# Optimization experiments

Measured on AMD Instinct MI355X. Metric: run time of the kernel, lower is better.

Reference implementation:

```python
import jax, jax.numpy as jnp
import numpy as np

B, H, L, P = 16, 256, 4096, 64  # batch, d_input, seq len (= kernel_size), d_state
R_MIN, R_MAX = 0.9, 1.0         # strong_stability, weak_stability (discrete reservoir radii)


def _as_complex(x):
    # torch.view_as_complex equivalent: trailing dim 2 = (real, imag)
    return x[..., 0] + 1j * x[..., 1]


def setup_inputs() -> dict:
    key = jax.random.key(0)
    ks = jax.random.split(key, 6)
    u = jax.random.normal(ks[0], (B, H, L), jnp.float32)
    C = jax.random.normal(ks[1], (H, P, 2), jnp.float32)       # complex (H,P) as view_as_real
    D = jax.random.normal(ks[2], (H, H), jnp.float32)
    B_bar = jax.random.normal(ks[3], (P, H, 2), jnp.float32)   # complex (P,H) as view_as_real
    # DiscreteStateReservoir: eigenvalues with |lambda| in [strong, weak), uniform phase
    radius = jax.random.uniform(ks[4], (P,), jnp.float32, R_MIN, R_MAX)
    theta = jax.random.uniform(ks[5], (P,), jnp.float32, 0.0, 2.0 * np.pi)
    Lambda_bar = jnp.stack([radius * jnp.cos(theta), radius * jnp.sin(theta)], axis=-1)
    powers = jnp.arange(L, dtype=jnp.float32)
    return {"u": u, "C": C, "D": D, "B_bar": B_bar, "Lambda_bar": Lambda_bar, "powers": powers}


def reference(u, C, D, B_bar, Lambda_bar, powers):
    Cc = _as_complex(C)            # (H, P) complex64
    Bc = _as_complex(B_bar)        # (P, H) complex64
    Lc = _as_complex(Lambda_bar)   # (P,)   complex64
    # Vandermonde: (P, L) = Lambda_bar[p] ** powers[l]
    vand = Lc[:, None] ** powers[None, :]
    # einsum('hp,ph->hp') is elementwise C[h,p]*B_bar[p,h]; then contract over p
    kernel = jnp.einsum('hp,pl->hl', Cc * Bc.T, vand)            # (H, L) complex64
    # circular FFT convolution along L
    y = jnp.fft.ifft(jnp.fft.fft(u, axis=-1) * jnp.fft.fft(kernel, axis=-1)[None], axis=-1)
    # einsum('hh,bhl->bhl', D, u) uses only diag(D)
    y = y.real + jnp.diagonal(D)[None, :, None] * u
    return jnp.tanh(y)
```

## Files before the change

### kernel.cpp

```cpp
#include <hip/hip_runtime.h>
#include <cmath>

#define NF 4096
#define PI2F 6.2831853071795864769f

typedef float2 cf;

__device__ __forceinline__ cf cmulf(cf a, cf b){
  return make_float2(fmaf(a.x, b.x, -(a.y*b.y)), fmaf(a.x, b.y, a.y*b.x));
}
__device__ __forceinline__ cf cadd(cf a, cf b){ return make_float2(a.x+b.x, a.y+b.y); }
__device__ __forceinline__ cf csub(cf a, cf b){ return make_float2(a.x-b.x, a.y-b.y); }

__device__ __forceinline__ int phys(int i){ return i + (i >> 3); }

__device__ __forceinline__ int rev8(int i){
  return ((i & 7) << 9) | (((i >> 3) & 7) << 6) | (((i >> 6) & 7) << 3) | ((i >> 9) & 7);
}

template<int INV>
__device__ __forceinline__ void dft8(cf* v){
  const float HF = 0.7071067811865476f;
  cf e0,e1,e2,e3,o0,o1,o2,o3;
  {
    cf t0 = cadd(v[0], v[4]);
    cf t1 = csub(v[0], v[4]);
    cf t2 = cadd(v[2], v[6]);
    cf t3 = csub(v[2], v[6]);
    e0 = cadd(t0,t2); e2 = csub(t0,t2);
    if (!INV){ e1 = make_float2(t1.x+t3.y, t1.y-t3.x); e3 = make_float2(t1.x-t3.y, t1.y+t3.x); }
    else     { e1 = make_float2(t1.x-t3.y, t1.y+t3.x); e3 = make_float2(t1.x+t3.y, t1.y-t3.x); }
  }
  {
    cf t0 = cadd(v[1], v[5]);
    cf t1 = csub(v[1], v[5]);
    cf t2 = cadd(v[3], v[7]);
    cf t3 = csub(v[3], v[7]);
    o0 = cadd(t0,t2); o2 = csub(t0,t2);
    if (!INV){ o1 = make_float2(t1.x+t3.y, t1.y-t3.x); o3 = make_float2(t1.x-t3.y, t1.y+t3.x); }
    else     { o1 = make_float2(t1.x-t3.y, t1.y+t3.x); o3 = make_float2(t1.x+t3.y, t1.y-t3.x); }
  }
  cf w1, w2, w3;
  if (!INV){
    w1 = make_float2(HF*(o1.x + o1.y), HF*(o1.y - o1.x));
    w2 = make_float2(o2.y, -o2.x);
    w3 = make_float2(HF*(o3.y - o3.x), -HF*(o3.x + o3.y));
  } else {
    w1 = make_float2(HF*(o1.x - o1.y), HF*(o1.y + o1.x));
    w2 = make_float2(-o2.y, o2.x);
    w3 = make_float2(-HF*(o3.x + o3.y), HF*(o3.x - o3.y));
  }
  v[0] = cadd(e0,o0); v[4] = csub(e0,o0);
  v[1] = cadd(e1,w1); v[5] = csub(e1,w1);
  v[2] = cadd(e2,w2); v[6] = csub(e2,w2);
  v[3] = cadd(e3,w3); v[7] = csub(e3,w3);
}

__device__ __forceinline__ void twiddle8(cf* v, float ang){
  float s, c;
  __sincosf(ang, &s, &c);
  cf T1 = make_float2(c, s);
  cf T2 = cmulf(T1, T1);
  cf T3 = cmulf(T2, T1);
  cf T4 = cmulf(T2, T2);
  cf T5 = cmulf(T3, T2);
  cf T6 = cmulf(T3, T3);
  cf T7 = cmulf(T4, T3);
  v[1] = cmulf(v[1], T1); v[2] = cmulf(v[2], T2); v[3] = cmulf(v[3], T3);
  v[4] = cmulf(v[4], T4); v[5] = cmulf(v[5], T5); v[6] = cmulf(v[6], T6);
  v[7] = cmulf(v[7], T7);
}

__device__ __forceinline__ float fast_tanh(float x){
  float e = __expf(2.0f*x);
  return 1.0f - __fdividef(2.0f, e + 1.0f);
}

__global__ void k_vand(const float* __restrict__ Lam, cf* __restrict__ vand){
  int gid = blockIdx.x*256 + threadIdx.x;
  int p = gid >> 12;
  int l = gid & 4095;
  float lr = Lam[2*p], li = Lam[2*p+1];
  double r2 = (double)lr*(double)lr + (double)li*(double)li;
  double lg = 0.5 * log2(r2);
  double tt = atan2((double)li, (double)lr) * 0.15915494309189535;
  double dl = (double)l;
  float mag = exp2f((float)(dl * lg));
  double ph = dl * tt;
  ph -= floor(ph);
  float s, c;
  sincospif((float)(2.0*ph), &s, &c);
  vand[gid] = make_float2(mag*c, mag*s);
}

__global__ __launch_bounds__(512,4) void k_kr(
    const float* __restrict__ C, const float* __restrict__ Bb,
    const cf* __restrict__ vand, float* __restrict__ Kr){
  __shared__ cf Wsh[8][64];
  __shared__ cf Vt[16][512];
  const int t = threadIdx.x;
  const int hg = blockIdx.x >> 3;
  const int ls = blockIdx.x & 7;
  const int h0 = hg*8;
  const int l0 = ls*512;
  {
    int hl = t >> 6, p = t & 63;
    int h = h0 + hl;
    cf cc = ((const cf*)C)[h*64 + p];
    cf bb = ((const cf*)Bb)[p*256 + h];
    Wsh[hl][p] = cmulf(cc, bb);
  }
  float acc[8] = {0,0,0,0,0,0,0,0};
  const int hl = t >> 6;
  const int lane = t & 63;
  for (int pc = 0; pc < 4; ++pc){
    __syncthreads();
    const float4* src = (const float4*)vand;
#pragma unroll
    for (int j = 0; j < 8; ++j){
      int li = j*512 + t;
      int rp = li >> 8;
      int colf4 = li & 255;
      ((float4*)Vt)[li] = src[(size_t)(pc*16 + rp)*2048 + (l0 >> 1) + colf4];
    }
    __syncthreads();
#pragma unroll
    for (int p = 0; p < 16; ++p){
      cf w = Wsh[hl][pc*16 + p];
#pragma unroll
      for (int j = 0; j < 8; ++j){
        cf vv = Vt[p][lane + 64*j];
        acc[j] = fmaf(w.x, vv.x, fmaf(-w.y, vv.y, acc[j]));
      }
    }
  }
  float* dst = Kr + (size_t)(h0 + hl)*NF + l0;
#pragma unroll
  for (int j = 0; j < 8; ++j) dst[lane + 64*j] = acc[j];
}

__global__ __launch_bounds__(512,4) void k_fftkr(
    const float* __restrict__ Kr, const float* __restrict__ D, cf* __restrict__ M){
  __shared__ cf X[4608];
  const int t = threadIdx.x;
  const int h0 = blockIdx.x*2, h1 = h0 + 1;
  const float* kr0 = Kr + (size_t)h0*NF;
  const float* kr1 = Kr + (size_t)h1*NF;
  cf v[8];
#pragma unroll
  for (int q = 0; q < 8; ++q) v[q] = make_float2(kr0[t + 512*q], kr1[t + 512*q]);
  dft8<0>(v);
  twiddle8(v, -(PI2F/4096.0f)*(float)t);
#pragma unroll
  for (int r = 0; r < 8; ++r) X[phys(t + 512*r)] = v[r];
  __syncthreads();
  const int b2 = ((t >> 6) << 9) | (t & 63);
#pragma unroll
  for (int q = 0; q < 8; ++q) v[q] = X[phys(b2 + 64*q)];
  dft8<0>(v);
  twiddle8(v, -(PI2F/512.0f)*(float)(t & 63));
#pragma unroll
  for (int r = 0; r < 8; ++r) X[phys(b2 + 64*r)] = v[r];
  __syncthreads();
  const int b3 = ((t >> 3) << 6) | (t & 7);
#pragma unroll
  for (int q = 0; q < 8; ++q) v[q] = X[phys(b3 + 8*q)];
  dft8<0>(v);
  twiddle8(v, -(PI2F/64.0f)*(float)(t & 7));
#pragma unroll
  for (int r = 0; r < 8; ++r) X[phys(b3 + 8*r)] = v[r];
  __syncthreads();
#pragma unroll
  for (int q = 0; q < 8; ++q) v[q] = X[phys(8*t + q)];
  dft8<0>(v);
#pragma unroll
  for (int q = 0; q < 8; ++q) X[phys(8*t + q)] = v[q];
  __syncthreads();
  const float dd0 = D[h0*256 + h0];
  const float dd1 = D[h1*256 + h1];
  const float invN = 1.0f/4096.0f;
  float4* M0f = (float4*)(M + (size_t)h0*NF);
  float4* M1f = (float4*)(M + (size_t)h1*NF);
#pragma unroll
  for (int j = 0; j < 4; ++j){
    cf e0[2], e1[2];
#pragma unroll
    for (int s = 0; s < 2; ++s){
      int idx = 8*t + 2*j + s;
      cf Z = v[2*j + s];
      int k    = rev8(idx);
      int kc   = (4096 - k) & 4095;
      int pidx = rev8(kc);
      cf Zp = X[phys(pidx)];
      e0[s] = make_float2((0.5f*(Z.x + Zp.x) + dd0)*invN, 0.5f*(Z.y - Zp.y)*invN);
      e1[s] = make_float2((0.5f*(Z.y + Zp.y) + dd1)*invN, 0.5f*(Zp.x - Z.x)*invN);
    }
    M0f[4*t + j] = make_float4(e0[0].x, e0[0].y, e0[1].x, e0[1].y);
    M1f[4*t + j] = make_float4(e1[0].x, e1[0].y, e1[1].x, e1[1].y);
  }
}

__global__ __launch_bounds__(512,8) void k_main(
    const float* __restrict__ u, const cf* __restrict__ M, float* __restrict__ out){
  __shared__ cf X[4608];
  const int t  = threadIdx.x;
  const int h  = blockIdx.x >> 3;
  const int pr = blockIdx.x & 7;
  const size_t row0 = ((size_t)pr*256 + h)*(size_t)NF;
  const size_t row1 = row0 + (size_t)8*256*NF;
  const float* u0 = u + row0;
  const float* u1 = u + row1;
  cf v[8];
#pragma unroll
  for (int q = 0; q < 8; ++q) v[q] = make_float2(u0[t + 512*q], u1[t + 512*q]);
  dft8<0>(v);
  twiddle8(v, -(PI2F/4096.0f)*(float)t);
#pragma unroll
  for (int r = 0; r < 8; ++r) X[phys(t + 512*r)] = v[r];
  __syncthreads();
  const int b2 = ((t >> 6) << 9) | (t & 63);
#pragma unroll
  for (int q = 0; q < 8; ++q) v[q] = X[phys(b2 + 64*q)];
  dft8<0>(v);
  twiddle8(v, -(PI2F/512.0f)*(float)(t & 63));
#pragma unroll
  for (int r = 0; r < 8; ++r) X[phys(b2 + 64*r)] = v[r];
  __syncthreads();
  const int b3 = ((t >> 3) << 6) | (t & 7);
#pragma unroll
  for (int q = 0; q < 8; ++q) v[q] = X[phys(b3 + 8*q)];
  dft8<0>(v);
  twiddle8(v, -(PI2F/64.0f)*(float)(t & 7));
#pragma unroll
  for (int r = 0; r < 8; ++r) X[phys(b3 + 8*r)] = v[r];
  __syncthreads();
  float4 mf0, mf1;
  {
    const float4* Mr = (const float4*)(M + (size_t)h*NF + 8*t);
    mf0 = Mr[0]; mf1 = Mr[1];
  }
#pragma unroll
  for (int q = 0; q < 8; ++q) v[q] = X[phys(8*t + q)];
  dft8<0>(v);
  {
    const float4* Mr = (const float4*)(M + (size_t)h*NF + 8*t);
    float4 f2 = Mr[2], f3 = Mr[3];
    v[0] = cmulf(v[0], make_float2(mf0.x, mf0.y));
    v[1] = cmulf(v[1], make_float2(mf0.z, mf0.w));
    v[2] = cmulf(v[2], make_float2(mf1.x, mf1.y));
    v[3] = cmulf(v[3], make_float2(mf1.z, mf1.w));
    v[4] = cmulf(v[4], make_float2(f2.x, f2.y));
    v[5] = cmulf(v[5], make_float2(f2.z, f2.w));
    v[6] = cmulf(v[6], make_float2(f3.x, f3.y));
    v[7] = cmulf(v[7], make_float2(f3.z, f3.w));
  }
  dft8<1>(v);
#pragma unroll
  for (int q = 0; q < 8; ++q) X[phys(8*t + q)] = v[q];
  __syncthreads();
#pragma unroll
  for (int r = 0; r < 8; ++r) v[r] = X[phys(b3 + 8*r)];
  twiddle8(v, (PI2F/64.0f)*(float)(t & 7));
  dft8<1>(v);
#pragma unroll
  for (int q = 0; q < 8; ++q) X[phys(b3 + 8*q)] = v[q];
  __syncthreads();
#pragma unroll
  for (int r = 0; r < 8; ++r) v[r] = X[phys(b2 + 64*r)];
  twiddle8(v, (PI2F/512.0f)*(float)(t & 63));
  dft8<1>(v);
#pragma unroll
  for (int q = 0; q < 8; ++q) X[phys(b2 + 64*q)] = v[q];
  __syncthreads();
#pragma unroll
  for (int r = 0; r < 8; ++r) v[r] = X[phys(t + 512*r)];
  twiddle8(v, (PI2F/4096.0f)*(float)t);
  dft8<1>(v);
  float* o0 = out + row0;
  float* o1 = out + row1;
#pragma unroll
  for (int q = 0; q < 8; ++q){
    o0[t + 512*q] = fast_tanh(v[q].x);
    o1[t + 512*q] = fast_tanh(v[q].y);
  }
}

extern "C" void kernel_launch(void* const* d_in, const int* in_sizes, int n_in,
                              void* d_out, int out_size, void* d_ws, size_t ws_size,
                              hipStream_t stream){
  const float* u   = (const float*)d_in[0];
  const float* C   = (const float*)d_in[1];
  const float* D   = (const float*)d_in[2];
  const float* Bb  = (const float*)d_in[3];
  const float* Lam = (const float*)d_in[4];
  float* out = (float*)d_out;
  char* ws = (char*)d_ws;
  cf*    M    = (cf*)ws;
  cf*    vand = (cf*)(ws + (size_t)(8u << 20));
  float* Kr   = (float*)(ws + (size_t)(10u << 20));

  k_vand <<<dim3(1024), dim3(256), 0, stream>>>(Lam, vand);
  k_kr   <<<dim3(256),  dim3(512), 0, stream>>>(C, Bb, vand, Kr);
  k_fftkr<<<dim3(128),  dim3(512), 0, stream>>>(Kr, D, M);
  k_main <<<dim3(2048), dim3(512), 0, stream>>>(u, M, out);
}
```

Baseline: 72.55 us.

## Compute kernel spectrum analytically via geometric series, drop kernel FFT

Replaces the Vandermonde table, time-domain kernel reduction and kernel FFT with a closed-form geometric-series DFT per eigenvalue. The per-eigenvalue spectrum factors are precomputed in double precision in bit-reversed order, then reduced over P directly into the frequency-domain multiplier M. This removes one kernel launch and the kernel FFT pass. The twiddle powers are now generated by a Chebyshev recurrence instead of repeated complex multiplies. The cost is extra double-precision transcendental work in the table kernel and a larger float4 table read.

```diff
diff --git a/kernel.cpp b/kernel.cpp
--- a/kernel.cpp
+++ b/kernel.cpp
@@ -12,7 +12,7 @@
 __device__ __forceinline__ cf cadd(cf a, cf b){ return make_float2(a.x+b.x, a.y+b.y); }
 __device__ __forceinline__ cf csub(cf a, cf b){ return make_float2(a.x-b.x, a.y-b.y); }
 
-__device__ __forceinline__ int phys(int i){ return i + (i >> 3); }
+__device__ __forceinline__ int phys8(int i){ return i + (i >> 3); }
 
 __device__ __forceinline__ int rev8(int i){
   return ((i & 7) << 9) | (((i >> 3) & 7) << 6) | (((i >> 6) & 7) << 3) | ((i >> 9) & 7);
@@ -59,16 +59,15 @@
 __device__ __forceinline__ void twiddle8(cf* v, float ang){
   float s, c;
   __sincosf(ang, &s, &c);
-  cf T1 = make_float2(c, s);
-  cf T2 = cmulf(T1, T1);
-  cf T3 = cmulf(T2, T1);
-  cf T4 = cmulf(T2, T2);
-  cf T5 = cmulf(T3, T2);
-  cf T6 = cmulf(T3, T3);
-  cf T7 = cmulf(T4, T3);
-  v[1] = cmulf(v[1], T1); v[2] = cmulf(v[2], T2); v[3] = cmulf(v[3], T3);
-  v[4] = cmulf(v[4], T4); v[5] = cmulf(v[5], T5); v[6] = cmulf(v[6], T6);
-  v[7] = cmulf(v[7], T7);
+  float c2 = 2.0f * c;
+  cf T[8];
+  T[1] = make_float2(c, s);
+  T[2] = make_float2(fmaf(c2, c, -1.0f), c2 * s);
+#pragma unroll
+  for (int r = 3; r < 8; ++r)
+    T[r] = make_float2(fmaf(c2, T[r-1].x, -T[r-2].x), fmaf(c2, T[r-1].y, -T[r-2].y));
+#pragma unroll
+  for (int r = 1; r < 8; ++r) v[r] = cmulf(v[r], T[r]);
 }
 
 __device__ __forceinline__ float fast_tanh(float x){
@@ -76,127 +75,98 @@
   return 1.0f - __fdividef(2.0f, e + 1.0f);
 }
 
-__global__ void k_vand(const float* __restrict__ Lam, cf* __restrict__ vand){
+__global__ void k_geo(const float* __restrict__ Lam, float4* __restrict__ tab){
   int gid = blockIdx.x*256 + threadIdx.x;
   int p = gid >> 12;
-  int l = gid & 4095;
-  float lr = Lam[2*p], li = Lam[2*p+1];
-  double r2 = (double)lr*(double)lr + (double)li*(double)li;
-  double lg = 0.5 * log2(r2);
-  double tt = atan2((double)li, (double)lr) * 0.15915494309189535;
-  double dl = (double)l;
-  float mag = exp2f((float)(dl * lg));
-  double ph = dl * tt;
-  ph -= floor(ph);
-  float s, c;
-  sincospif((float)(2.0*ph), &s, &c);
-  vand[gid] = make_float2(mag*c, mag*s);
-}
-
-__global__ __launch_bounds__(512,4) void k_kr(
+  int w = gid & 4095;
+  int k = rev8(w);
+  double lr = (double)Lam[2*p], li = (double)Lam[2*p+1];
+  double r2 = lr*lr + li*li;
+  double r  = sqrt(r2);
+  double tt = atan2(li, lr) * 0.15915494309189535;
+  double rN = exp2(4096.0 * (0.5 * log2(r2)));
+  double pN = 4096.0 * tt;
+  pN -= floor(pN);
+  double sN, cN;
+  sincospi(2.0*pN, &sN, &cN);
+  double numr = 1.0 - rN*cN;
+  double numi =     - rN*sN;
+  double ph1 = tt - (double)k * (1.0/4096.0);
+  double s1, c1; sincospi(2.0*ph1, &s1, &c1);
+  double d1r = 1.0 - r*c1, d1i = -r*s1;
+  double inv1 = 1.0/(d1r*d1r + d1i*d1i);
+  double g1r = (numr*d1r + numi*d1i)*inv1;
+  double g1i = (numi*d1r - numr*d1i)*inv1;
+  double ph2 = tt + (double)k * (1.0/4096.0);
+  double s2, c2; sincospi(2.0*ph2, &s2, &c2);
+  double d2r = 1.0 - r*c2, d2i = -r*s2;
+  double inv2 = 1.0/(d2r*d2r + d2i*d2i);
+  double g2r = (numr*d2r + numi*d2i)*inv2;
+  double g2i = (numi*d2r - numr*d2i)*inv2;
+  const double hN = 0.5/4096.0;
+  double Ar  =  (g1r + g2r)*hN, Ai  = (g1i - g2i)*hN;
+  double B2r = -(g1i + g2i)*hN, B2i = (g1r - g2r)*hN;
+  tab[(size_t)p*4096 + w] = make_float4((float)Ar, (float)Ai, (float)B2r, (float)B2i);
+}
+
+__global__ __launch_bounds__(512,4) void k_red(
     const float* __restrict__ C, const float* __restrict__ Bb,
-    const cf* __restrict__ vand, float* __restrict__ Kr){
-  __shared__ cf Wsh[8][64];
-  __shared__ cf Vt[16][512];
-  const int t = threadIdx.x;
-  const int hg = blockIdx.x >> 3;
-  const int ls = blockIdx.x & 7;
-  const int h0 = hg*8;
-  const int l0 = ls*512;
-  {
-    int hl = t >> 6, p = t & 63;
+    const float4* __restrict__ tab, const float* __restrict__ D,
+    cf* __restrict__ M){
+  __shared__ cf Wsh[32][64];
+  __shared__ float4 Tt[8][128];
+  const int t  = threadIdx.x;
+  const int hg = blockIdx.x >> 5;
+  const int ls = blockIdx.x & 31;
+  const int h0 = hg*32;
+  const int w0 = ls*128;
+#pragma unroll
+  for (int e = 0; e < 4; ++e){
+    int idx = e*512 + t;
+    int hl = idx >> 6, p = idx & 63;
     int h = h0 + hl;
     cf cc = ((const cf*)C)[h*64 + p];
     cf bb = ((const cf*)Bb)[p*256 + h];
     Wsh[hl][p] = cmulf(cc, bb);
   }
-  float acc[8] = {0,0,0,0,0,0,0,0};
-  const int hl = t >> 6;
+  const int wave = t >> 6;
   const int lane = t & 63;
-  for (int pc = 0; pc < 4; ++pc){
+  const int hh = wave*4;
+  float accr[2][4] = {{0,0,0,0},{0,0,0,0}};
+  float acci[2][4] = {{0,0,0,0},{0,0,0,0}};
+  for (int pc = 0; pc < 8; ++pc){
     __syncthreads();
-    const float4* src = (const float4*)vand;
-#pragma unroll
-    for (int j = 0; j < 8; ++j){
-      int li = j*512 + t;
-      int rp = li >> 8;
-      int colf4 = li & 255;
-      ((float4*)Vt)[li] = src[(size_t)(pc*16 + rp)*2048 + (l0 >> 1) + colf4];
+#pragma unroll
+    for (int e = 0; e < 2; ++e){
+      int idx = e*512 + t;
+      int row = idx >> 7, col = idx & 127;
+      Tt[row][col] = tab[(size_t)(pc*8 + row)*4096 + w0 + col];
     }
     __syncthreads();
 #pragma unroll
-    for (int p = 0; p < 16; ++p){
-      cf w = Wsh[hl][pc*16 + p];
-#pragma unroll
-      for (int j = 0; j < 8; ++j){
-        cf vv = Vt[p][lane + 64*j];
-        acc[j] = fmaf(w.x, vv.x, fmaf(-w.y, vv.y, acc[j]));
+    for (int p = 0; p < 8; ++p){
+      cf Wc[4];
+#pragma unroll
+      for (int h = 0; h < 4; ++h) Wc[h] = Wsh[hh + h][pc*8 + p];
+#pragma unroll
+      for (int j = 0; j < 2; ++j){
+        float4 f = Tt[p][lane + 64*j];
+#pragma unroll
+        for (int h = 0; h < 4; ++h){
+          accr[j][h] = fmaf(Wc[h].x, f.x, fmaf(Wc[h].y, f.z, accr[j][h]));
+          acci[j][h] = fmaf(Wc[h].x, f.y, fmaf(Wc[h].y, f.w, acci[j][h]));
+        }
       }
     }
   }
-  float* dst = Kr + (size_t)(h0 + hl)*NF + l0;
-#pragma unroll
-  for (int j = 0; j < 8; ++j) dst[lane + 64*j] = acc[j];
-}
-
-__global__ __launch_bounds__(512,4) void k_fftkr(
-    const float* __restrict__ Kr, const float* __restrict__ D, cf* __restrict__ M){
-  __shared__ cf X[4608];
-  const int t = threadIdx.x;
-  const int h0 = blockIdx.x*2, h1 = h0 + 1;
-  const float* kr0 = Kr + (size_t)h0*NF;
-  const float* kr1 = Kr + (size_t)h1*NF;
-  cf v[8];
-#pragma unroll
-  for (int q = 0; q < 8; ++q) v[q] = make_float2(kr0[t + 512*q], kr1[t + 512*q]);
-  dft8<0>(v);
-  twiddle8(v, -(PI2F/4096.0f)*(float)t);
-#pragma unroll
-  for (int r = 0; r < 8; ++r) X[phys(t + 512*r)] = v[r];
-  __syncthreads();
-  const int b2 = ((t >> 6) << 9) | (t & 63);
-#pragma unroll
-  for (int q = 0; q < 8; ++q) v[q] = X[phys(b2 + 64*q)];
-  dft8<0>(v);
-  twiddle8(v, -(PI2F/512.0f)*(float)(t & 63));
-#pragma unroll
-  for (int r = 0; r < 8; ++r) X[phys(b2 + 64*r)] = v[r];
-  __syncthreads();
-  const int b3 = ((t >> 3) << 6) | (t & 7);
-#pragma unroll
-  for (int q = 0; q < 8; ++q) v[q] = X[phys(b3 + 8*q)];
-  dft8<0>(v);
-  twiddle8(v, -(PI2F/64.0f)*(float)(t & 7));
-#pragma unroll
-  for (int r = 0; r < 8; ++r) X[phys(b3 + 8*r)] = v[r];
-  __syncthreads();
-#pragma unroll
-  for (int q = 0; q < 8; ++q) v[q] = X[phys(8*t + q)];
-  dft8<0>(v);
-#pragma unroll
-  for (int q = 0; q < 8; ++q) X[phys(8*t + q)] = v[q];
-  __syncthreads();
-  const float dd0 = D[h0*256 + h0];
-  const float dd1 = D[h1*256 + h1];
   const float invN = 1.0f/4096.0f;
-  float4* M0f = (float4*)(M + (size_t)h0*NF);
-  float4* M1f = (float4*)(M + (size_t)h1*NF);
-#pragma unroll
-  for (int j = 0; j < 4; ++j){
-    cf e0[2], e1[2];
-#pragma unroll
-    for (int s = 0; s < 2; ++s){
-      int idx = 8*t + 2*j + s;
-      cf Z = v[2*j + s];
-      int k    = rev8(idx);
-      int kc   = (4096 - k) & 4095;
-      int pidx = rev8(kc);
-      cf Zp = X[phys(pidx)];
-      e0[s] = make_float2((0.5f*(Z.x + Zp.x) + dd0)*invN, 0.5f*(Z.y - Zp.y)*invN);
-      e1[s] = make_float2((0.5f*(Z.y + Zp.y) + dd1)*invN, 0.5f*(Zp.x - Z.x)*invN);
-    }
-    M0f[4*t + j] = make_float4(e0[0].x, e0[0].y, e0[1].x, e0[1].y);
-    M1f[4*t + j] = make_float4(e1[0].x, e1[0].y, e1[1].x, e1[1].y);
+#pragma unroll
+  for (int h = 0; h < 4; ++h){
+    int hq = h0 + hh + h;
+    float dd = D[hq*256 + hq] * invN;
+#pragma unroll
+    for (int j = 0; j < 2; ++j)
+      M[(size_t)hq*NF + w0 + lane + 64*j] = make_float2(accr[j][h] + dd, acci[j][h]);
   }
 }
 
@@ -216,23 +186,23 @@
   dft8<0>(v);
   twiddle8(v, -(PI2F/4096.0f)*(float)t);
 #pragma unroll
-  for (int r = 0; r < 8; ++r) X[phys(t + 512*r)] = v[r];
+  for (int r = 0; r < 8; ++r) X[phys8(t + 512*r)] = v[r];
   __syncthreads();
   const int b2 = ((t >> 6) << 9) | (t & 63);
 #pragma unroll
-  for (int q = 0; q < 8; ++q) v[q] = X[phys(b2 + 64*q)];
+  for (int q = 0; q < 8; ++q) v[q] = X[phys8(b2 + 64*q)];
   dft8<0>(v);
   twiddle8(v, -(PI2F/512.0f)*(float)(t & 63));
 #pragma unroll
-  for (int r = 0; r < 8; ++r) X[phys(b2 + 64*r)] = v[r];
+  for (int r = 0; r < 8; ++r) X[phys8(b2 + 64*r)] = v[r];
   __syncthreads();
   const int b3 = ((t >> 3) << 6) | (t & 7);
 #pragma unroll
-  for (int q = 0; q < 8; ++q) v[q] = X[phys(b3 + 8*q)];
+  for (int q = 0; q < 8; ++q) v[q] = X[phys8(b3 + 8*q)];
   dft8<0>(v);
   twiddle8(v, -(PI2F/64.0f)*(float)(t & 7));
 #pragma unroll
-  for (int r = 0; r < 8; ++r) X[phys(b3 + 8*r)] = v[r];
+  for (int r = 0; r < 8; ++r) X[phys8(b3 + 8*r)] = v[r];
   __syncthreads();
   float4 mf0, mf1;
   {
@@ -240,7 +210,7 @@
     mf0 = Mr[0]; mf1 = Mr[1];
   }
 #pragma unroll
-  for (int q = 0; q < 8; ++q) v[q] = X[phys(8*t + q)];
+  for (int q = 0; q < 8; ++q) v[q] = X[phys8(8*t + q)];
   dft8<0>(v);
   {
     const float4* Mr = (const float4*)(M + (size_t)h*NF + 8*t);
@@ -256,24 +226,24 @@
   }
   dft8<1>(v);
 #pragma unroll
-  for (int q = 0; q < 8; ++q) X[phys(8*t + q)] = v[q];
-  __syncthreads();
-#pragma unroll
-  for (int r = 0; r < 8; ++r) v[r] = X[phys(b3 + 8*r)];
+  for (int q = 0; q < 8; ++q) X[phys8(8*t + q)] = v[q];
+  __syncthreads();
+#pragma unroll
+  for (int r = 0; r < 8; ++r) v[r] = X[phys8(b3 + 8*r)];
   twiddle8(v, (PI2F/64.0f)*(float)(t & 7));
   dft8<1>(v);
 #pragma unroll
-  for (int q = 0; q < 8; ++q) X[phys(b3 + 8*q)] = v[q];
-  __syncthreads();
-#pragma unroll
-  for (int r = 0; r < 8; ++r) v[r] = X[phys(b2 + 64*r)];
+  for (int q = 0; q < 8; ++q) X[phys8(b3 + 8*q)] = v[q];
+  __syncthreads();
+#pragma unroll
+  for (int r = 0; r < 8; ++r) v[r] = X[phys8(b2 + 64*r)];
   twiddle8(v, (PI2F/512.0f)*(float)(t & 63));
   dft8<1>(v);
 #pragma unroll
-  for (int q = 0; q < 8; ++q) X[phys(b2 + 64*q)] = v[q];
-  __syncthreads();
-#pragma unroll
-  for (int r = 0; r < 8; ++r) v[r] = X[phys(t + 512*r)];
+  for (int q = 0; q < 8; ++q) X[phys8(b2 + 64*q)] = v[q];
+  __syncthreads();
+#pragma unroll
+  for (int r = 0; r < 8; ++r) v[r] = X[phys8(t + 512*r)];
   twiddle8(v, (PI2F/4096.0f)*(float)t);
   dft8<1>(v);
   float* o0 = out + row0;
@@ -295,12 +265,10 @@
   const float* Lam = (const float*)d_in[4];
   float* out = (float*)d_out;
   char* ws = (char*)d_ws;
-  cf*    M    = (cf*)ws;
-  cf*    vand = (cf*)(ws + (size_t)(8u << 20));
-  float* Kr   = (float*)(ws + (size_t)(10u << 20));
-
-  k_vand <<<dim3(1024), dim3(256), 0, stream>>>(Lam, vand);
-  k_kr   <<<dim3(256),  dim3(512), 0, stream>>>(C, Bb, vand, Kr);
-  k_fftkr<<<dim3(128),  dim3(512), 0, stream>>>(Kr, D, M);
-  k_main <<<dim3(2048), dim3(512), 0, stream>>>(u, M, out);
-}
+  cf*     M   = (cf*)ws;
+  float4* tab = (float4*)(ws + (size_t)(8u << 20));
+
+  k_geo <<<dim3(1024), dim3(256), 0, stream>>>(Lam, tab);
+  k_red <<<dim3(256),  dim3(512), 0, stream>>>(C, Bb, tab, D, M);
+  k_main<<<dim3(2048), dim3(512), 0, stream>>>(u, M, out);
+}
```

New measurement: 64.04 us. 11.7% less time.
